# Performance work log

Measured on AMD Instinct MI355X. Metric: run time of the kernel, lower is better.

## Reference

```python
import jax, jax.numpy as jnp
import numpy as np
from jax import lax

N_EMBED, N_HEAD, N_EXPERTS, TOP_K = 1024, 16, 8, 2
D_FF = 4 * N_EMBED
HEAD = N_EMBED // N_HEAD
LN_EPS = 1e-5


def _layernorm(x, gamma, beta):
    mu = jnp.mean(x, axis=-1, keepdims=True)
    var = jnp.var(x, axis=-1, keepdims=True)
    return (x - mu) * lax.rsqrt(var + LN_EPS) * gamma + beta


def setup_inputs() -> dict:
    key = jax.random.key(0)
    ks = jax.random.split(key, 16)
    B, T = 2, 2048
    s = 0.02
    return {
        "x": jax.random.normal(ks[0], (B, T, N_EMBED), jnp.float32),
        "noise": jax.random.normal(ks[1], (B, T, N_EXPERTS), jnp.float32),
        "gamma1": jnp.ones((N_EMBED,), jnp.float32),
        "beta1": jnp.zeros((N_EMBED,), jnp.float32),
        "gamma2": jnp.ones((N_EMBED,), jnp.float32),
        "beta2": jnp.zeros((N_EMBED,), jnp.float32),
        "w_qkv": jax.random.normal(ks[2], (N_EMBED, 3 * N_EMBED), jnp.float32) * s,
        "w_out": jax.random.normal(ks[3], (N_EMBED, N_EMBED), jnp.float32) * s,
        "w_route": jax.random.normal(ks[4], (N_EMBED, N_EXPERTS), jnp.float32) * s,
        "b_route": jnp.zeros((N_EXPERTS,), jnp.float32),
        "w_noise": jax.random.normal(ks[5], (N_EMBED, N_EXPERTS), jnp.float32) * s,
        "b_noise": jnp.zeros((N_EXPERTS,), jnp.float32),
        "w1": jax.random.normal(ks[6], (N_EXPERTS, N_EMBED, D_FF), jnp.float32) * s,
        "b1": jnp.zeros((N_EXPERTS, D_FF), jnp.float32),
        "w2": jax.random.normal(ks[7], (N_EXPERTS, D_FF, N_EMBED), jnp.float32) * s,
        "b2": jnp.zeros((N_EXPERTS, N_EMBED), jnp.float32),
    }


def _attention(h, w_qkv, w_out):
    B, T, C = h.shape
    qkv = (h @ w_qkv).reshape(B, T, 3, N_HEAD, HEAD)
    q, k, v = qkv[:, :, 0], qkv[:, :, 1], qkv[:, :, 2]  # (B,T,H,hd)
    scores = jnp.einsum("bthd,bshd->bhts", q, k) / jnp.sqrt(jnp.float32(HEAD))
    attn = jax.nn.softmax(scores, axis=-1)
    out = jnp.einsum("bhts,bshd->bthd", attn, v)  # (B,T,H,hd)
    # faithful reproduction of the original permute/reshape/permute sequence
    out = jnp.transpose(out, (0, 2, 1, 3)).reshape(B, C, T)
    out = jnp.transpose(out, (0, 2, 1))  # (B,T,C)
    return out @ w_out


def _sparse_moe(h, noise, w_route, b_route, w_noise, b_noise, w1, b1, w2, b2):
    B, T, C = h.shape
    N = B * T
    flat = h.reshape(N, C)
    logits = flat @ w_route + b_route
    noise_logits = flat @ w_noise + b_noise
    noisy = logits + noise.reshape(N, N_EXPERTS) * jax.nn.softplus(noise_logits)
    full_probs = jax.nn.softmax(noisy, axis=-1)
    top_vals, top_idx = lax.top_k(noisy, TOP_K)  # (N,k)
    gates = jax.nn.softmax(top_vals, axis=-1)
    dense_gates = jnp.zeros((N, N_EXPERTS), flat.dtype).at[
        jnp.arange(N)[:, None], top_idx
    ].set(gates)
    cap = (N * TOP_K) // N_EXPERTS  # expert capacity, capacity_factor=1.0
    updates = jnp.zeros_like(flat)
    for i in range(N_EXPERTS):
        mask = (top_idx == i).any(axis=-1)  # (N,)
        order = jnp.argsort((~mask).astype(jnp.int32), stable=True)
        idx = order[:cap]
        valid = mask[idx]
        xi = flat[idx]  # (cap,C)
        hid = jax.nn.relu(xi @ w1[i] + b1[i])
        yo = hid @ w2[i] + b2[i]
        g = dense_gates[idx, i] * valid.astype(flat.dtype)
        updates = updates.at[idx].add(yo * g[:, None])
    moe_out = updates.reshape(B, T, C)
    entropy = -jnp.sum(full_probs * jnp.log(full_probs + 1e-8), axis=-1)
    return moe_out, entropy.mean()


def reference(x, noise, gamma1, beta1, gamma2, beta2, w_qkv, w_out,
              w_route, b_route, w_noise, b_noise, w1, b1, w2, b2):
    x = x + _attention(_layernorm(x, gamma1, beta1), w_qkv, w_out)
    moe_out, entropy_loss = _sparse_moe(_layernorm(x, gamma2, beta2), noise,
                                        w_route, b_route, w_noise, b_noise,
                                        w1, b1, w2, b2)
    return x + moe_out, entropy_loss
```

## Files before the change

kernel.cpp:

```cpp
#include <hip/hip_runtime.h>
#include <hip/hip_bf16.h>


#define TT   2048
#define NTOK 4096
#define CE   1024
#define DFF  4096
#define NE   8
#define CAP  1024

typedef __bf16 bf16;
typedef __attribute__((ext_vector_type(8))) bf16 bf16x8;
typedef __attribute__((ext_vector_type(4))) bf16 bf16x4;
typedef __attribute__((ext_vector_type(4))) float f32x4;

typedef __attribute__((address_space(1))) const void* as1_t;
typedef __attribute__((address_space(3))) void* as3_t;
__device__ __forceinline__ void gll16(const void* g, void* l) {
  __builtin_amdgcn_global_load_lds((as1_t)g, (as3_t)l, 16, 0, 0);
}

__device__ __forceinline__ void split2(float v, bf16& h, bf16& l) {
  h = (bf16)v;
  l = (bf16)(v - (float)h);
}

__global__ void zero_k(float* zp) { zp[threadIdx.x] = 0.f; }

template <bool LO>
__global__ __launch_bounds__(256) void wsplit_k(const float* __restrict__ W,
                                                bf16* __restrict__ Th,
                                                bf16* __restrict__ Tl,
                                                int K, int N, long sW, long sT) {
  __shared__ float tile[64][65];
  const int e = blockIdx.z;
  const float* Wb = W + (long)e * sW;
  bf16* Thb = Th + (long)e * sT;
  bf16* Tlb = LO ? Tl + (long)e * sT : nullptr;
  const int k0 = blockIdx.y * 64, n0 = blockIdx.x * 64;
  const int tx = threadIdx.x & 15, ty = threadIdx.x >> 4;
#pragma unroll
  for (int i = 0; i < 4; i++) {
    int kk = ty + i * 16;
    float4 v = *(const float4*)&Wb[(long)(k0 + kk) * N + n0 + tx * 4];
    tile[kk][tx * 4 + 0] = v.x;
    tile[kk][tx * 4 + 1] = v.y;
    tile[kk][tx * 4 + 2] = v.z;
    tile[kk][tx * 4 + 3] = v.w;
  }
  __syncthreads();
#pragma unroll
  for (int i = 0; i < 4; i++) {
    int nn = ty + i * 16;
    bf16x4 hv, lv;
#pragma unroll
    for (int j = 0; j < 4; j++) {
      float v = tile[tx * 4 + j][nn];
      bf16 h, l;
      split2(v, h, l);
      hv[j] = h;
      lv[j] = l;
    }
    long o = (long)(n0 + nn) * K + k0 + tx * 4;
    *(bf16x4*)(Thb + o) = hv;
    if (LO) *(bf16x4*)(Tlb + o) = lv;
  }
}

__global__ __launch_bounds__(256) void ln_k(const float* __restrict__ in,
                                            const float* __restrict__ g,
                                            const float* __restrict__ b,
                                            float* __restrict__ outf,
                                            bf16* __restrict__ outh,
                                            bf16* __restrict__ outl) {
  int row = blockIdx.x, tid = threadIdx.x;
  const float* xr = in + (long)row * CE;
  float v[4];
  float s = 0.f, s2 = 0.f;
#pragma unroll
  for (int i = 0; i < 4; i++) {
    v[i] = xr[tid + 256 * i];
    s += v[i];
    s2 += v[i] * v[i];
  }
#pragma unroll
  for (int o = 32; o; o >>= 1) {
    s += __shfl_xor(s, o);
    s2 += __shfl_xor(s2, o);
  }
  __shared__ float rs[4], rs2[4];
  int w = tid >> 6, lane = tid & 63;
  if (lane == 0) { rs[w] = s; rs2[w] = s2; }
  __syncthreads();
  s = rs[0] + rs[1] + rs[2] + rs[3];
  s2 = rs2[0] + rs2[1] + rs2[2] + rs2[3];
  float mu = s * (1.f / CE);
  float var = s2 * (1.f / CE) - mu * mu;
  float rstd = rsqrtf(var + 1e-5f);
  long rb = (long)row * CE;
#pragma unroll
  for (int i = 0; i < 4; i++) {
    int c = tid + 256 * i;
    float y = (v[i] - mu) * rstd * g[c] + b[c];
    if (outf) outf[rb + c] = y;
    bf16 h, l;
    split2(y, h, l);
    outh[rb + c] = h;
    outl[rb + c] = l;
  }
}

template <int NPASS, int EPI, bool AGATHER>
__global__ __launch_bounds__(256, 2) void gemm_k(
    const bf16* __restrict__ Ah, const bf16* __restrict__ Al,
    const bf16* __restrict__ BTh, const bf16* __restrict__ BTl,
    void* __restrict__ O0, void* __restrict__ O1, void* __restrict__ O2,
    void* __restrict__ O3, int M, int N, int K,
    const float* __restrict__ resid, const float* __restrict__ bias,
    const int* __restrict__ tokens, const int* __restrict__ counts,
    long sA, long sBT, long sC, int sBias, const bf16* __restrict__ zp) {
  constexpr int NS = (NPASS > 1) ? 2 : 1;
  __shared__ bf16 As[NS][128 * 32];
  __shared__ bf16 Bs[NS][128 * 32];
  const int e = blockIdx.z;
  const int n0 = blockIdx.x * 128, m0 = blockIdx.y * 128;
  const int tid = threadIdx.x;
  const int w = tid >> 6, lane = tid & 63, lm = lane & 15, qd = lane >> 4;
  const int wm = (w & 1) * 64, wn = (w >> 1) * 64;

  const bf16* Ab = Ah + (long)e * sA;
  const bf16* AbL = (NS > 1) ? Al + (long)e * sA : nullptr;
  const bf16* Bb = BTh + (long)e * sBT;
  const bf16* BbL = (NS > 1) ? BTl + (long)e * sBT : nullptr;

  const int srow0 = w * 32 + (lane >> 2);
  const int kc = (lane & 3) * 8;
  const int ldsB0 = (w * 128) * 8;
  const int ldsB1 = (w * 128 + 64) * 8;

  const bf16 *aP0, *aP1;
  int aStep0 = 32, aStep1 = 32;
  if (AGATHER) {
    int cnt = counts[e];
    int r0 = m0 + srow0, r1 = r0 + 16;
    int t0 = (r0 < cnt) ? tokens[e * CAP + r0] : -1;
    int t1 = (r1 < cnt) ? tokens[e * CAP + r1] : -1;
    aP0 = (t0 >= 0) ? Ab + (long)t0 * K + kc : zp + kc;
    aP1 = (t1 >= 0) ? Ab + (long)t1 * K + kc : zp + kc;
    if (t0 < 0) aStep0 = 0;
    if (t1 < 0) aStep1 = 0;
  } else {
    aP0 = Ab + (long)(m0 + srow0) * K + kc;
    aP1 = Ab + (long)(m0 + srow0 + 16) * K + kc;
  }
  const bf16* bP0 = Bb + (long)(n0 + srow0) * K + kc;
  const bf16* bP1 = Bb + (long)(n0 + srow0 + 16) * K + kc;
  const bf16* aP0L = nullptr; const bf16* aP1L = nullptr;
  const bf16* bP0L = nullptr; const bf16* bP1L = nullptr;
  if (NS > 1) {
    aP0L = AbL + (aP0 - Ab);
    aP1L = AbL + (aP1 - Ab);
    bP0L = BbL + (bP0 - Bb);
    bP1L = BbL + (bP1 - Bb);
  }

  f32x4 acc[4][4];
#pragma unroll
  for (int i = 0; i < 4; i++)
#pragma unroll
    for (int j = 0; j < 4; j++) acc[i][j] = (f32x4){0.f, 0.f, 0.f, 0.f};

  for (int k0 = 0; k0 < K; k0 += 32) {
    gll16(aP0, (char*)&As[0][0] + ldsB0 * 2);
    gll16(aP1, (char*)&As[0][0] + ldsB1 * 2);
    gll16(bP0, (char*)&Bs[0][0] + ldsB0 * 2);
    gll16(bP1, (char*)&Bs[0][0] + ldsB1 * 2);
    if (NS > 1) {
      gll16(aP0L, (char*)&As[1][0] + ldsB0 * 2);
      gll16(aP1L, (char*)&As[1][0] + ldsB1 * 2);
      gll16(bP0L, (char*)&Bs[1][0] + ldsB0 * 2);
      gll16(bP1L, (char*)&Bs[1][0] + ldsB1 * 2);
      aP0L += aStep0; aP1L += aStep1; bP0L += 32; bP1L += 32;
    }
    aP0 += aStep0; aP1 += aStep1; bP0 += 32; bP1 += 32;
    __syncthreads();
    bf16x8 af[NS][4], bfv[NS][4];
#pragma unroll
    for (int j = 0; j < 4; j++)
#pragma unroll
      for (int s = 0; s < NS; s++) {
        af[s][j] = *(const bf16x8*)&As[s][(wm + j * 16 + lm) * 32 + qd * 8];
        bfv[s][j] = *(const bf16x8*)&Bs[s][(wn + j * 16 + lm) * 32 + qd * 8];
      }
#pragma unroll
    for (int i = 0; i < 4; i++)
#pragma unroll
      for (int j = 0; j < 4; j++) {
        acc[i][j] = __builtin_amdgcn_mfma_f32_16x16x32_bf16(
            af[0][i], bfv[0][j], acc[i][j], 0, 0, 0);
        if (NPASS > 1) {
          acc[i][j] = __builtin_amdgcn_mfma_f32_16x16x32_bf16(
              af[0][i], bfv[1][j], acc[i][j], 0, 0, 0);
          acc[i][j] = __builtin_amdgcn_mfma_f32_16x16x32_bf16(
              af[1][i], bfv[0][j], acc[i][j], 0, 0, 0);
        }
      }
    __syncthreads();
  }
#pragma unroll
  for (int i = 0; i < 4; i++)
#pragma unroll
    for (int j = 0; j < 4; j++) {
      long row = m0 + wm + i * 16 + qd * 4;
      long col = n0 + wn + j * 16 + lm;
      if (EPI == 0) {
        if (col < 2048) {
          bf16* qh = (bf16*)O0;
          bf16* ql = (bf16*)O1;
#pragma unroll
          for (int r = 0; r < 4; r++) {
            bf16 h, l;
            split2(acc[i][j][r], h, l);
            qh[(row + r) * 2048 + col] = h;
            ql[(row + r) * 2048 + col] = l;
          }
        } else {
          long vd = col - 2048;
          long bb = row >> 11, t = row & 2047;
          bf16x4 hv, lv;
#pragma unroll
          for (int r = 0; r < 4; r++) {
            bf16 h, l;
            split2(acc[i][j][r], h, l);
            hv[r] = h;
            lv[r] = l;
          }
          long o = (bb * 1024 + vd) * (long)TT + t;
          *(bf16x4*)((bf16*)O2 + o) = hv;
          *(bf16x4*)((bf16*)O3 + o) = lv;
        }
      } else if (EPI == 1) {
        float* outp = (float*)O0;
#pragma unroll
        for (int r = 0; r < 4; r++)
          outp[(row + r) * N + col] = resid[(row + r) * N + col] + acc[i][j][r];
      } else if (EPI == 2) {
        bf16* hid = (bf16*)O0;
        float bv = bias[e * sBias + col];
#pragma unroll
        for (int r = 0; r < 4; r++) {
          float t = acc[i][j][r] + bv;
          hid[(long)e * sC + (row + r) * (long)N + col] =
              (bf16)(t > 0.f ? t : 0.f);
        }
      } else {
        float* eo = (float*)O0;
        float bv = bias[e * sBias + col];
#pragma unroll
        for (int r = 0; r < 4; r++)
          eo[(long)e * sC + (row + r) * (long)N + col] = acc[i][j][r] + bv;
      }
    }
}

__global__ __launch_bounds__(256, 2) void attn_k(
    const bf16* __restrict__ qkvh, const bf16* __restrict__ qkvl,
    const bf16* __restrict__ VTh, const bf16* __restrict__ VTl,
    bf16* __restrict__ attn_h, bf16* __restrict__ attn_l) {
  const int qt = blockIdx.x, h = blockIdx.y, b = blockIdx.z;
  const int tid = threadIdx.x, w = tid >> 6, lane = tid & 63;
  const int lm = lane & 15, qd = lane >> 4;
  __shared__ bf16 Ks[2][64 * 64];
  __shared__ bf16 Vs[2][64 * 64];
  __shared__ bf16 Ps[4][2][32][72];
  const long bb = (long)b * TT;

  bf16x8 qfh[2][2], qfl[2][2];
#pragma unroll
  for (int i = 0; i < 2; i++) {
    long qrow = (bb + qt * 128 + w * 32 + i * 16 + lm) * 2048 + h * 64;
#pragma unroll
    for (int kk = 0; kk < 2; kk++) {
      qfh[i][kk] = *(const bf16x8*)(qkvh + qrow + kk * 32 + qd * 8);
      qfl[i][kk] = *(const bf16x8*)(qkvl + qrow + kk * 32 + qd * 8);
    }
  }

  const int ktok = tid >> 3, dc = tid & 7;
  const int kws = ktok * 64 + ((dc ^ (ktok & 7)) * 8);
  const long gK0 = (bb + ktok) * 2048 + 1024 + h * 64 + dc * 8;
  const int vd = tid >> 3, tc = tid & 7;
  const int vws = vd * 64 + ((tc ^ (vd & 7)) * 8);
  const long gV0 = ((long)b * 1024 + h * 64 + vd) * (long)TT + tc * 8;

  const bf16* pKh = qkvh + gK0;
  const bf16* pKl = qkvl + gK0;
  const bf16* pVh = VTh + gV0;
  const bf16* pVl = VTl + gV0;

  float4 rkh0, rkh1, rkl0, rkl1, rvh0, rvh1, rvl0, rvl1;
#define LOADT()                                     \
  do {                                              \
    rkh0 = *(const float4*)(pKh);                   \
    rkh1 = *(const float4*)(pKh + 32 * 2048);       \
    rkl0 = *(const float4*)(pKl);                   \
    rkl1 = *(const float4*)(pKl + 32 * 2048);       \
    rvh0 = *(const float4*)(pVh);                   \
    rvh1 = *(const float4*)(pVh + 32 * TT);         \
    rvl0 = *(const float4*)(pVl);                   \
    rvl1 = *(const float4*)(pVl + 32 * TT);         \
  } while (0)
  LOADT();

  float m_i[2][4], l_i[2][4];
  f32x4 o[2][4];
#pragma unroll
  for (int i = 0; i < 2; i++)
#pragma unroll
    for (int r = 0; r < 4; r++) { m_i[i][r] = -1e30f; l_i[i][r] = 0.f; }
#pragma unroll
  for (int i = 0; i < 2; i++)
#pragma unroll
    for (int nt = 0; nt < 4; nt++) o[i][nt] = (f32x4){0.f, 0.f, 0.f, 0.f};

  const float SC = 0.125f * 1.4426950408889634f;

  for (int kt = 0; kt < TT / 64; kt++) {
    __syncthreads();
    *(float4*)&Ks[0][kws] = rkh0;
    *(float4*)&Ks[0][kws + 32 * 64] = rkh1;
    *(float4*)&Ks[1][kws] = rkl0;
    *(float4*)&Ks[1][kws + 32 * 64] = rkl1;
    *(float4*)&Vs[0][vws] = rvh0;
    *(float4*)&Vs[0][vws + 32 * 64] = rvh1;
    *(float4*)&Vs[1][vws] = rvl0;
    *(float4*)&Vs[1][vws + 32 * 64] = rvl1;
    if (kt != TT / 64 - 1) {
      pKh += 64 * 2048; pKl += 64 * 2048; pVh += 64; pVl += 64;
      LOADT();
    }
    __syncthreads();
    f32x4 sv[2][4];
#pragma unroll
    for (int i = 0; i < 2; i++)
#pragma unroll
      for (int nt = 0; nt < 4; nt++) {
        f32x4 s4 = (f32x4){0.f, 0.f, 0.f, 0.f};
        int tok = nt * 16 + lm;
#pragma unroll
        for (int kk = 0; kk < 2; kk++) {
          int slot = ((kk * 4 + qd) ^ (lm & 7)) * 8;
          bf16x8 kh = *(const bf16x8*)&Ks[0][tok * 64 + slot];
          bf16x8 kl = *(const bf16x8*)&Ks[1][tok * 64 + slot];
          s4 = __builtin_amdgcn_mfma_f32_16x16x32_bf16(qfh[i][kk], kh, s4, 0, 0, 0);
          s4 = __builtin_amdgcn_mfma_f32_16x16x32_bf16(qfh[i][kk], kl, s4, 0, 0, 0);
          s4 = __builtin_amdgcn_mfma_f32_16x16x32_bf16(qfl[i][kk], kh, s4, 0, 0, 0);
        }
        sv[i][nt] = s4 * SC;
      }
    float alpha[2][4];
#pragma unroll
    for (int i = 0; i < 2; i++)
#pragma unroll
      for (int r = 0; r < 4; r++) {
        float mx = fmaxf(fmaxf(sv[i][0][r], sv[i][1][r]),
                         fmaxf(sv[i][2][r], sv[i][3][r]));
#pragma unroll
        for (int d = 8; d; d >>= 1) mx = fmaxf(mx, __shfl_xor(mx, d));
        float mn = fmaxf(m_i[i][r], mx);
        alpha[i][r] = __builtin_exp2f(m_i[i][r] - mn);
        float rsum = 0.f;
#pragma unroll
        for (int nt = 0; nt < 4; nt++) {
          float p = __builtin_exp2f(sv[i][nt][r] - mn);
          sv[i][nt][r] = p;
          rsum += p;
        }
#pragma unroll
        for (int d = 8; d; d >>= 1) rsum += __shfl_xor(rsum, d);
        l_i[i][r] = l_i[i][r] * alpha[i][r] + rsum;
        m_i[i][r] = mn;
      }
#pragma unroll
    for (int i = 0; i < 2; i++)
#pragma unroll
      for (int nt = 0; nt < 4; nt++)
#pragma unroll
        for (int r = 0; r < 4; r++) {
          bf16 hh, ll;
          split2(sv[i][nt][r], hh, ll);
          Ps[w][0][i * 16 + qd * 4 + r][nt * 16 + lm] = hh;
          Ps[w][1][i * 16 + qd * 4 + r][nt * 16 + lm] = ll;
        }
#pragma unroll
    for (int i = 0; i < 2; i++)
#pragma unroll
      for (int nt = 0; nt < 4; nt++)
#pragma unroll
        for (int r = 0; r < 4; r++) o[i][nt][r] *= alpha[i][r];
#pragma unroll
    for (int i = 0; i < 2; i++)
#pragma unroll
      for (int kc = 0; kc < 2; kc++) {
        bf16x8 ph = *(const bf16x8*)&Ps[w][0][i * 16 + lm][kc * 32 + qd * 8];
        bf16x8 pl = *(const bf16x8*)&Ps[w][1][i * 16 + lm][kc * 32 + qd * 8];
#pragma unroll
        for (int nt = 0; nt < 4; nt++) {
          int drow = nt * 16 + lm;
          int slot = ((kc * 4 + qd) ^ (lm & 7)) * 8;
          bf16x8 vh = *(const bf16x8*)&Vs[0][drow * 64 + slot];
          bf16x8 vl = *(const bf16x8*)&Vs[1][drow * 64 + slot];
          o[i][nt] = __builtin_amdgcn_mfma_f32_16x16x32_bf16(ph, vh, o[i][nt], 0, 0, 0);
          o[i][nt] = __builtin_amdgcn_mfma_f32_16x16x32_bf16(ph, vl, o[i][nt], 0, 0, 0);
          o[i][nt] = __builtin_amdgcn_mfma_f32_16x16x32_bf16(pl, vh, o[i][nt], 0, 0, 0);
        }
      }
  }
#pragma unroll
  for (int i = 0; i < 2; i++)
#pragma unroll
    for (int nt = 0; nt < 4; nt++)
#pragma unroll
      for (int r = 0; r < 4; r++) {
        int t = qt * 128 + w * 32 + i * 16 + qd * 4 + r;
        int d = nt * 16 + lm;
        int ttn = (t & 31) * 64 + d;
        int c = h * 64 + (t >> 5);
        float v = o[i][nt][r] / l_i[i][r];
        bf16 hh, ll;
        split2(v, hh, ll);
        long idx = (bb + ttn) * (long)CE + c;
        attn_h[idx] = hh;
        attn_l[idx] = ll;
      }
#undef LOADT
}

__global__ __launch_bounds__(64) void route_k(
    const float* __restrict__ hln, const float* __restrict__ noise,
    const float* __restrict__ wr, const float* __restrict__ br,
    const float* __restrict__ wn, const float* __restrict__ bn,
    int* __restrict__ top_e, float* __restrict__ gates,
    float* __restrict__ entb) {
  int n = blockIdx.x, lane = threadIdx.x;
  const float* hr = hln + (long)n * CE;
  float aR[NE], aN[NE];
#pragma unroll
  for (int e = 0; e < NE; e++) { aR[e] = 0.f; aN[e] = 0.f; }
  for (int i = lane; i < CE; i += 64) {
    float hv = hr[i];
#pragma unroll
    for (int e = 0; e < NE; e++) {
      aR[e] += hv * wr[i * NE + e];
      aN[e] += hv * wn[i * NE + e];
    }
  }
#pragma unroll
  for (int e = 0; e < NE; e++)
#pragma unroll
    for (int d = 32; d; d >>= 1) {
      aR[e] += __shfl_xor(aR[e], d);
      aN[e] += __shfl_xor(aN[e], d);
    }
  if (lane == 0) {
    float ns[NE];
#pragma unroll
    for (int e = 0; e < NE; e++) {
      float lg = aR[e] + br[e];
      float nl = aN[e] + bn[e];
      float sp = (nl > 20.f) ? nl : log1pf(expf(nl));
      ns[e] = lg + noise[(long)n * NE + e] * sp;
    }
    int i0 = 0;
#pragma unroll
    for (int e = 1; e < NE; e++)
      if (ns[e] > ns[i0]) i0 = e;
    int i1 = (i0 == 0) ? 1 : 0;
#pragma unroll
    for (int e = 0; e < NE; e++)
      if (e != i0 && ns[e] > ns[i1]) i1 = e;
    float v0 = ns[i0], v1 = ns[i1];
    float e1v = expf(v1 - v0);
    float inv2 = 1.f / (1.f + e1v);
    top_e[2 * n] = i0;
    top_e[2 * n + 1] = i1;
    gates[2 * n] = inv2;
    gates[2 * n + 1] = e1v * inv2;
    float ssum = 0.f, p[NE];
#pragma unroll
    for (int e = 0; e < NE; e++) {
      p[e] = expf(ns[e] - v0);
      ssum += p[e];
    }
    float is = 1.f / ssum, ent = 0.f;
#pragma unroll
    for (int e = 0; e < NE; e++) {
      float pe = p[e] * is;
      ent -= pe * logf(pe + 1e-8f);
    }
    entb[n] = ent;
  }
}

__global__ __launch_bounds__(256) void assign_k(const int* __restrict__ top_e,
                                                int* __restrict__ tokens,
                                                int* __restrict__ slots,
                                                int* __restrict__ counts) {
  int e = blockIdx.x, tid = threadIdx.x, w = tid >> 6, lane = tid & 63;
  __shared__ int wtot[4];
  int basec = 0;
  for (int c = 0; c < 16; c++) {
    int n = c * 256 + tid;
    int e0 = top_e[2 * n], e1 = top_e[2 * n + 1];
    bool flag = (e0 == e) || (e1 == e);
    int rank = (e0 == e) ? 0 : 1;
    unsigned long long mask = __ballot(flag);
    int pre = __popcll(mask & ((1ull << lane) - 1ull));
    if (lane == 0) wtot[w] = __popcll(mask);
    __syncthreads();
    int wbase = basec;
    for (int i = 0; i < w; i++) wbase += wtot[i];
    if (flag) {
      int slot = wbase + pre;
      if (slot < CAP) {
        tokens[e * CAP + slot] = n;
        slots[2 * n + rank] = slot;
      } else {
        slots[2 * n + rank] = -1;
      }
    }
    int tot = wtot[0] + wtot[1] + wtot[2] + wtot[3];
    __syncthreads();
    basec += tot;
  }
  if (tid == 0) counts[e] = basec < CAP ? basec : CAP;
}

__global__ __launch_bounds__(256) void gather_k(
    float* __restrict__ outp, const float* __restrict__ eo,
    const int* __restrict__ top_e, const float* __restrict__ gates,
    const int* __restrict__ slots) {
  int n = blockIdx.x, tid = threadIdx.x;
  int e0 = top_e[2 * n], e1 = top_e[2 * n + 1];
  int s0 = slots[2 * n], s1 = slots[2 * n + 1];
  float g0 = gates[2 * n], g1 = gates[2 * n + 1];
  const float* r0 = (s0 >= 0) ? eo + ((long)e0 * CAP + s0) * CE : nullptr;
  const float* r1 = (s1 >= 0) ? eo + ((long)e1 * CAP + s1) * CE : nullptr;
  float* orow = outp + (long)n * CE;
  for (int i = tid; i < CE; i += 256) {
    float v = orow[i];
    if (r0) v += g0 * r0[i];
    if (r1) v += g1 * r1[i];
    orow[i] = v;
  }
}

__global__ __launch_bounds__(256) void entropy_k(const float* __restrict__ entb,
                                                 float* __restrict__ outp) {
  int tid = threadIdx.x;
  float s = 0.f;
  for (int i = tid; i < NTOK; i += 256) s += entb[i];
#pragma unroll
  for (int d = 32; d; d >>= 1) s += __shfl_xor(s, d);
  __shared__ float rs[4];
  int w = tid >> 6, lane = tid & 63;
  if (lane == 0) rs[w] = s;
  __syncthreads();
  if (tid == 0)
    outp[(long)NTOK * CE] = (rs[0] + rs[1] + rs[2] + rs[3]) * (1.f / NTOK);
}

extern "C" void kernel_launch(void* const* d_in, const int* in_sizes, int n_in,
                              void* d_out, int out_size, void* d_ws,
                              size_t ws_size, hipStream_t stream) {
  const float* x = (const float*)d_in[0];
  const float* noise = (const float*)d_in[1];
  const float* gamma1 = (const float*)d_in[2];
  const float* beta1 = (const float*)d_in[3];
  const float* gamma2 = (const float*)d_in[4];
  const float* beta2 = (const float*)d_in[5];
  const float* w_qkv = (const float*)d_in[6];
  const float* w_out = (const float*)d_in[7];
  const float* w_route = (const float*)d_in[8];
  const float* b_route = (const float*)d_in[9];
  const float* w_noise = (const float*)d_in[10];
  const float* b_noise = (const float*)d_in[11];
  const float* w1 = (const float*)d_in[12];
  const float* b1 = (const float*)d_in[13];
  const float* w2 = (const float*)d_in[14];
  const float* b2 = (const float*)d_in[15];
  float* out = (float*)d_out;

  char* ws = (char*)d_ws;
  size_t offA = 0;
  bf16* qkvh = (bf16*)(ws + offA);  offA += (size_t)NTOK * 2048 * 2;
  bf16* qkvl = (bf16*)(ws + offA);  offA += (size_t)NTOK * 2048 * 2;
  bf16* VTh = (bf16*)(ws + offA);   offA += (size_t)2 * 1024 * TT * 2;
  bf16* VTl = (bf16*)(ws + offA);   offA += (size_t)2 * 1024 * TT * 2;
  size_t attn_off = offA;
  bf16* attn_h = (bf16*)(ws + offA); offA += (size_t)NTOK * CE * 2;
  bf16* attn_l = (bf16*)(ws + offA); offA += (size_t)NTOK * CE * 2;
  bf16* hid = (bf16*)ws;
  float* h2f = (float*)(ws + attn_off);
  size_t szA = offA;
  size_t offB = szA;
  bf16* h1h = (bf16*)(ws + offB);    offB += (size_t)NTOK * CE * 2;
  bf16* h1l = (bf16*)(ws + offB);    offB += (size_t)NTOK * CE * 2;
  bf16* wqkvTh = (bf16*)(ws + offB); offB += (size_t)3072 * 1024 * 2;
  bf16* wqkvTl = (bf16*)(ws + offB); offB += (size_t)3072 * 1024 * 2;
  bf16* woutTh = (bf16*)(ws + offB); offB += (size_t)1024 * 1024 * 2;
  bf16* woutTl = (bf16*)(ws + offB); offB += (size_t)1024 * 1024 * 2;
  bf16* h2h = (bf16*)(ws + szA);
  bf16* h2l = (bf16*)(ws + szA + (size_t)NTOK * CE * 2);
  float* eo = (float*)(ws + szA);
  size_t offC = offB;
  bf16* w1T = (bf16*)(ws + offC);
  bf16* w2T = w1T;
  offC += (size_t)NE * DFF * CE * 2;
  size_t offS = offC;
  int* top_e = (int*)(ws + offS);   offS += (size_t)NTOK * 2 * 4;
  float* gates = (float*)(ws + offS); offS += (size_t)NTOK * 2 * 4;
  int* slots = (int*)(ws + offS);   offS += (size_t)NTOK * 2 * 4;
  int* toks = (int*)(ws + offS);    offS += (size_t)NE * CAP * 4;
  int* counts = (int*)(ws + offS);  offS += 256;
  float* entb = (float*)(ws + offS); offS += (size_t)NTOK * 4;
  float* zp = (float*)(ws + offS);  offS += 256;
  if (offS > ws_size) return;

  zero_k<<<1, 64, 0, stream>>>(zp);
  wsplit_k<true><<<dim3(48, 16, 1), 256, 0, stream>>>(w_qkv, wqkvTh, wqkvTl,
                                                      1024, 3072, 0, 0);
  wsplit_k<true><<<dim3(16, 16, 1), 256, 0, stream>>>(w_out, woutTh, woutTl,
                                                      1024, 1024, 0, 0);
  wsplit_k<false><<<dim3(64, 16, 8), 256, 0, stream>>>(
      w1, w1T, nullptr, 1024, DFF, (long)CE * DFF, (long)DFF * CE);
  ln_k<<<NTOK, 256, 0, stream>>>(x, gamma1, beta1, nullptr, h1h, h1l);
  gemm_k<3, 0, false><<<dim3(24, 32, 1), 256, 0, stream>>>(
      h1h, h1l, wqkvTh, wqkvTl, qkvh, qkvl, VTh, VTl, NTOK, 3 * CE, CE,
      nullptr, nullptr, nullptr, nullptr, 0, 0, 0, 0, (const bf16*)zp);
  attn_k<<<dim3(16, 16, 2), 256, 0, stream>>>(qkvh, qkvl, VTh, VTl, attn_h,
                                              attn_l);
  gemm_k<3, 1, false><<<dim3(8, 32, 1), 256, 0, stream>>>(
      attn_h, attn_l, woutTh, woutTl, out, nullptr, nullptr, nullptr, NTOK, CE,
      CE, x, nullptr, nullptr, nullptr, 0, 0, 0, 0, (const bf16*)zp);
  ln_k<<<NTOK, 256, 0, stream>>>(out, gamma2, beta2, h2f, h2h, h2l);
  route_k<<<NTOK, 64, 0, stream>>>(h2f, noise, w_route, b_route, w_noise,
                                   b_noise, top_e, gates, entb);
  assign_k<<<NE, 256, 0, stream>>>(top_e, toks, slots, counts);
  gemm_k<1, 2, true><<<dim3(DFF / 128, CAP / 128, NE), 256, 0, stream>>>(
      h2h, nullptr, w1T, nullptr, hid, nullptr, nullptr, nullptr, CAP, DFF, CE,
      nullptr, b1, toks, counts, 0, (long)DFF * CE, (long)CAP * DFF, DFF,
      (const bf16*)zp);
  wsplit_k<false><<<dim3(16, 64, 8), 256, 0, stream>>>(
      w2, w2T, nullptr, DFF, CE, (long)DFF * CE, (long)CE * DFF);
  gemm_k<1, 3, false><<<dim3(CE / 128, CAP / 128, NE), 256, 0, stream>>>(
      hid, nullptr, w2T, nullptr, eo, nullptr, nullptr, nullptr, CAP, CE, DFF,
      nullptr, b2, nullptr, nullptr, (long)CAP * DFF, (long)CE * DFF,
      (long)CAP * CE, CE, (const bf16*)zp);
  gather_k<<<NTOK, 256, 0, stream>>>(out, eo, top_e, gates, slots);
  entropy_k<<<1, 256, 0, stream>>>(entb, out);
}
```

Measured before the change: 983.4 us.

## Fuse MoE combine into FFN2 epilogue, drop online softmax max, retile out-proj GEMM

Several changes land together. The second expert GEMM now scatters gated results straight into the output with atomicAdd, which removes the expert-output buffer and the separate gather kernel. Attention drops the running-max online softmax and exponentiates raw scaled scores, saving the max reductions and rescales but risking overflow for large logits. The V transpose/split moves out of the QKV GEMM epilogue into a new kernel, the out-projection GEMM uses 64-row tiles for more blocks, and the zero-init kernel is folded into the first layernorm.

```diff
diff --git a/kernel.cpp b/kernel.cpp
--- a/kernel.cpp
+++ b/kernel.cpp
@@ -24,8 +24,6 @@
   h = (bf16)v;
   l = (bf16)(v - (float)h);
 }
-
-__global__ void zero_k(float* zp) { zp[threadIdx.x] = 0.f; }
 
 template <bool LO>
 __global__ __launch_bounds__(256) void wsplit_k(const float* __restrict__ W,
@@ -67,13 +65,50 @@
   }
 }
 
+__global__ __launch_bounds__(256) void vsplit_k(const float* __restrict__ V,
+                                                bf16* __restrict__ Th,
+                                                bf16* __restrict__ Tl) {
+  __shared__ float tile[64][65];
+  const int b = blockIdx.z;
+  const int vd0 = blockIdx.x * 64, t0 = blockIdx.y * 64;
+  const int tx = threadIdx.x & 15, ty = threadIdx.x >> 4;
+#pragma unroll
+  for (int i = 0; i < 4; i++) {
+    int tt = ty + i * 16;
+    float4 v = *(const float4*)&V[((long)b * TT + t0 + tt) * 1024 + vd0 + tx * 4];
+    tile[tt][tx * 4 + 0] = v.x;
+    tile[tt][tx * 4 + 1] = v.y;
+    tile[tt][tx * 4 + 2] = v.z;
+    tile[tt][tx * 4 + 3] = v.w;
+  }
+  __syncthreads();
+#pragma unroll
+  for (int i = 0; i < 4; i++) {
+    int vd = ty + i * 16;
+    bf16x4 hv, lv;
+#pragma unroll
+    for (int j = 0; j < 4; j++) {
+      float v = tile[tx * 4 + j][vd];
+      bf16 h, l;
+      split2(v, h, l);
+      hv[j] = h;
+      lv[j] = l;
+    }
+    long o = ((long)b * 1024 + vd0 + vd) * (long)TT + t0 + tx * 4;
+    *(bf16x4*)(Th + o) = hv;
+    *(bf16x4*)(Tl + o) = lv;
+  }
+}
+
 __global__ __launch_bounds__(256) void ln_k(const float* __restrict__ in,
                                             const float* __restrict__ g,
                                             const float* __restrict__ b,
                                             float* __restrict__ outf,
                                             bf16* __restrict__ outh,
-                                            bf16* __restrict__ outl) {
+                                            bf16* __restrict__ outl,
+                                            float* __restrict__ zp) {
   int row = blockIdx.x, tid = threadIdx.x;
+  if (zp && row == 0 && tid < 64) zp[tid] = 0.f;
   const float* xr = in + (long)row * CE;
   float v[4];
   float s = 0.f, s2 = 0.f;
@@ -110,90 +145,100 @@
   }
 }
 
-template <int NPASS, int EPI, bool AGATHER>
+template <int NPASS, int EPI, bool AGATHER, int TM>
 __global__ __launch_bounds__(256, 2) void gemm_k(
     const bf16* __restrict__ Ah, const bf16* __restrict__ Al,
     const bf16* __restrict__ BTh, const bf16* __restrict__ BTl,
     void* __restrict__ O0, void* __restrict__ O1, void* __restrict__ O2,
-    void* __restrict__ O3, int M, int N, int K,
-    const float* __restrict__ resid, const float* __restrict__ bias,
-    const int* __restrict__ tokens, const int* __restrict__ counts,
+    int M, int N, int K, const float* __restrict__ resid,
+    const float* __restrict__ bias, const int* __restrict__ tokens,
+    const int* __restrict__ counts, const float* __restrict__ gslot,
     long sA, long sBT, long sC, int sBias, const bf16* __restrict__ zp) {
   constexpr int NS = (NPASS > 1) ? 2 : 1;
-  __shared__ bf16 As[NS][128 * 32];
+  constexpr int MI = TM / 32;
+  constexpr int AISS = TM / 64;
+  __shared__ bf16 As[NS][TM * 32];
   __shared__ bf16 Bs[NS][128 * 32];
   const int e = blockIdx.z;
-  const int n0 = blockIdx.x * 128, m0 = blockIdx.y * 128;
+  const int n0 = blockIdx.x * 128, m0 = blockIdx.y * TM;
   const int tid = threadIdx.x;
   const int w = tid >> 6, lane = tid & 63, lm = lane & 15, qd = lane >> 4;
-  const int wm = (w & 1) * 64, wn = (w >> 1) * 64;
+  const int wm = (w & 1) * (TM / 2), wn = (w >> 1) * 64;
 
   const bf16* Ab = Ah + (long)e * sA;
   const bf16* AbL = (NS > 1) ? Al + (long)e * sA : nullptr;
   const bf16* Bb = BTh + (long)e * sBT;
   const bf16* BbL = (NS > 1) ? BTl + (long)e * sBT : nullptr;
 
-  const int srow0 = w * 32 + (lane >> 2);
   const int kc = (lane & 3) * 8;
-  const int ldsB0 = (w * 128) * 8;
-  const int ldsB1 = (w * 128 + 64) * 8;
-
-  const bf16 *aP0, *aP1;
-  int aStep0 = 32, aStep1 = 32;
-  if (AGATHER) {
-    int cnt = counts[e];
-    int r0 = m0 + srow0, r1 = r0 + 16;
-    int t0 = (r0 < cnt) ? tokens[e * CAP + r0] : -1;
-    int t1 = (r1 < cnt) ? tokens[e * CAP + r1] : -1;
-    aP0 = (t0 >= 0) ? Ab + (long)t0 * K + kc : zp + kc;
-    aP1 = (t1 >= 0) ? Ab + (long)t1 * K + kc : zp + kc;
-    if (t0 < 0) aStep0 = 0;
-    if (t1 < 0) aStep1 = 0;
-  } else {
-    aP0 = Ab + (long)(m0 + srow0) * K + kc;
-    aP1 = Ab + (long)(m0 + srow0 + 16) * K + kc;
-  }
-  const bf16* bP0 = Bb + (long)(n0 + srow0) * K + kc;
-  const bf16* bP1 = Bb + (long)(n0 + srow0 + 16) * K + kc;
-  const bf16* aP0L = nullptr; const bf16* aP1L = nullptr;
-  const bf16* bP0L = nullptr; const bf16* bP1L = nullptr;
-  if (NS > 1) {
-    aP0L = AbL + (aP0 - Ab);
-    aP1L = AbL + (aP1 - Ab);
-    bP0L = BbL + (bP0 - Bb);
-    bP1L = BbL + (bP1 - Bb);
-  }
-
-  f32x4 acc[4][4];
-#pragma unroll
-  for (int i = 0; i < 4; i++)
+  int cnt = 0;
+  if (AGATHER || EPI == 3) cnt = counts[e];
+
+  const bf16* aP[AISS];
+  const bf16* aPL[AISS];
+  int aStep[AISS];
+  int ldsA[AISS];
+#pragma unroll
+  for (int ii = 0; ii < AISS; ii++) {
+    int sr = w * (TM / 4) + ii * 16 + (lane >> 2);
+    ldsA[ii] = (w * TM + ii * 64) * 8;
+    aStep[ii] = 32;
+    if (AGATHER) {
+      int gm = m0 + sr;
+      int tk = (gm < cnt) ? tokens[e * CAP + gm] : -1;
+      if (tk < 0) { aP[ii] = (const bf16*)zp + kc; aStep[ii] = 0; }
+      else aP[ii] = Ab + (long)tk * K + kc;
+    } else {
+      aP[ii] = Ab + (long)(m0 + sr) * K + kc;
+    }
+    aPL[ii] = (NS > 1) ? AbL + (aP[ii] - Ab) : nullptr;
+  }
+  const bf16* bP[2];
+  const bf16* bPL[2];
+  int ldsB[2];
+#pragma unroll
+  for (int ii = 0; ii < 2; ii++) {
+    int sr = w * 32 + ii * 16 + (lane >> 2);
+    ldsB[ii] = (w * 128 + ii * 64) * 8;
+    bP[ii] = Bb + (long)(n0 + sr) * K + kc;
+    bPL[ii] = (NS > 1) ? BbL + (bP[ii] - Bb) : nullptr;
+  }
+
+  f32x4 acc[MI][4];
+#pragma unroll
+  for (int i = 0; i < MI; i++)
 #pragma unroll
     for (int j = 0; j < 4; j++) acc[i][j] = (f32x4){0.f, 0.f, 0.f, 0.f};
 
   for (int k0 = 0; k0 < K; k0 += 32) {
-    gll16(aP0, (char*)&As[0][0] + ldsB0 * 2);
-    gll16(aP1, (char*)&As[0][0] + ldsB1 * 2);
-    gll16(bP0, (char*)&Bs[0][0] + ldsB0 * 2);
-    gll16(bP1, (char*)&Bs[0][0] + ldsB1 * 2);
-    if (NS > 1) {
-      gll16(aP0L, (char*)&As[1][0] + ldsB0 * 2);
-      gll16(aP1L, (char*)&As[1][0] + ldsB1 * 2);
-      gll16(bP0L, (char*)&Bs[1][0] + ldsB0 * 2);
-      gll16(bP1L, (char*)&Bs[1][0] + ldsB1 * 2);
-      aP0L += aStep0; aP1L += aStep1; bP0L += 32; bP1L += 32;
-    }
-    aP0 += aStep0; aP1 += aStep1; bP0 += 32; bP1 += 32;
+#pragma unroll
+    for (int ii = 0; ii < AISS; ii++) {
+      gll16(aP[ii], (char*)&As[0][0] + ldsA[ii] * 2);
+      if (NS > 1) gll16(aPL[ii], (char*)&As[1][0] + ldsA[ii] * 2);
+      aP[ii] += aStep[ii];
+      if (NS > 1) aPL[ii] += aStep[ii];
+    }
+#pragma unroll
+    for (int ii = 0; ii < 2; ii++) {
+      gll16(bP[ii], (char*)&Bs[0][0] + ldsB[ii] * 2);
+      if (NS > 1) gll16(bPL[ii], (char*)&Bs[1][0] + ldsB[ii] * 2);
+      bP[ii] += 32;
+      if (NS > 1) bPL[ii] += 32;
+    }
     __syncthreads();
-    bf16x8 af[NS][4], bfv[NS][4];
+    bf16x8 af[NS][MI], bfv[NS][4];
 #pragma unroll
     for (int j = 0; j < 4; j++)
 #pragma unroll
-      for (int s = 0; s < NS; s++) {
-        af[s][j] = *(const bf16x8*)&As[s][(wm + j * 16 + lm) * 32 + qd * 8];
+      for (int s = 0; s < NS; s++)
         bfv[s][j] = *(const bf16x8*)&Bs[s][(wn + j * 16 + lm) * 32 + qd * 8];
-      }
-#pragma unroll
-    for (int i = 0; i < 4; i++)
+#pragma unroll
+    for (int i = 0; i < MI; i++)
+#pragma unroll
+      for (int s = 0; s < NS; s++)
+        af[s][i] = *(const bf16x8*)&As[s][(wm + i * 16 + lm) * 32 + qd * 8];
+#pragma unroll
+    for (int i = 0; i < MI; i++)
 #pragma unroll
       for (int j = 0; j < 4; j++) {
         acc[i][j] = __builtin_amdgcn_mfma_f32_16x16x32_bf16(
@@ -208,7 +253,7 @@
     __syncthreads();
   }
 #pragma unroll
-  for (int i = 0; i < 4; i++)
+  for (int i = 0; i < MI; i++)
 #pragma unroll
     for (int j = 0; j < 4; j++) {
       long row = m0 + wm + i * 16 + qd * 4;
@@ -225,19 +270,10 @@
             ql[(row + r) * 2048 + col] = l;
           }
         } else {
+          float* vt = (float*)O2;
           long vd = col - 2048;
-          long bb = row >> 11, t = row & 2047;
-          bf16x4 hv, lv;
-#pragma unroll
-          for (int r = 0; r < 4; r++) {
-            bf16 h, l;
-            split2(acc[i][j][r], h, l);
-            hv[r] = h;
-            lv[r] = l;
-          }
-          long o = (bb * 1024 + vd) * (long)TT + t;
-          *(bf16x4*)((bf16*)O2 + o) = hv;
-          *(bf16x4*)((bf16*)O3 + o) = lv;
+#pragma unroll
+          for (int r = 0; r < 4; r++) vt[(row + r) * 1024 + vd] = acc[i][j][r];
         }
       } else if (EPI == 1) {
         float* outp = (float*)O0;
@@ -254,11 +290,17 @@
               (bf16)(t > 0.f ? t : 0.f);
         }
       } else {
-        float* eo = (float*)O0;
+        float* outp = (float*)O0;
         float bv = bias[e * sBias + col];
 #pragma unroll
-        for (int r = 0; r < 4; r++)
-          eo[(long)e * sC + (row + r) * (long)N + col] = acc[i][j][r] + bv;
+        for (int r = 0; r < 4; r++) {
+          long rr = row + r;
+          if (rr < cnt) {
+            int tok = tokens[e * CAP + rr];
+            float gv = gslot[e * CAP + rr];
+            atomicAdd(&outp[(long)tok * CE + col], gv * (acc[i][j][r] + bv));
+          }
+        }
       }
     }
 }
@@ -299,25 +341,25 @@
   const bf16* pVl = VTl + gV0;
 
   float4 rkh0, rkh1, rkl0, rkl1, rvh0, rvh1, rvl0, rvl1;
-#define LOADT()                                     \
-  do {                                              \
-    rkh0 = *(const float4*)(pKh);                   \
-    rkh1 = *(const float4*)(pKh + 32 * 2048);       \
-    rkl0 = *(const float4*)(pKl);                   \
-    rkl1 = *(const float4*)(pKl + 32 * 2048);       \
-    rvh0 = *(const float4*)(pVh);                   \
-    rvh1 = *(const float4*)(pVh + 32 * TT);         \
-    rvl0 = *(const float4*)(pVl);                   \
-    rvl1 = *(const float4*)(pVl + 32 * TT);         \
+#define LOADT()                               \
+  do {                                        \
+    rkh0 = *(const float4*)(pKh);             \
+    rkh1 = *(const float4*)(pKh + 32 * 2048); \
+    rkl0 = *(const float4*)(pKl);             \
+    rkl1 = *(const float4*)(pKl + 32 * 2048); \
+    rvh0 = *(const float4*)(pVh);             \
+    rvh1 = *(const float4*)(pVh + 32 * TT);   \
+    rvl0 = *(const float4*)(pVl);             \
+    rvl1 = *(const float4*)(pVl + 32 * TT);   \
   } while (0)
   LOADT();
 
-  float m_i[2][4], l_i[2][4];
+  float l_lane[2][4];
   f32x4 o[2][4];
 #pragma unroll
   for (int i = 0; i < 2; i++)
 #pragma unroll
-    for (int r = 0; r < 4; r++) { m_i[i][r] = -1e30f; l_i[i][r] = 0.f; }
+    for (int r = 0; r < 4; r++) l_lane[i][r] = 0.f;
 #pragma unroll
   for (int i = 0; i < 2; i++)
 #pragma unroll
@@ -344,78 +386,68 @@
 #pragma unroll
     for (int i = 0; i < 2; i++)
 #pragma unroll
-      for (int nt = 0; nt < 4; nt++) {
-        f32x4 s4 = (f32x4){0.f, 0.f, 0.f, 0.f};
-        int tok = nt * 16 + lm;
-#pragma unroll
-        for (int kk = 0; kk < 2; kk++) {
-          int slot = ((kk * 4 + qd) ^ (lm & 7)) * 8;
-          bf16x8 kh = *(const bf16x8*)&Ks[0][tok * 64 + slot];
-          bf16x8 kl = *(const bf16x8*)&Ks[1][tok * 64 + slot];
-          s4 = __builtin_amdgcn_mfma_f32_16x16x32_bf16(qfh[i][kk], kh, s4, 0, 0, 0);
-          s4 = __builtin_amdgcn_mfma_f32_16x16x32_bf16(qfh[i][kk], kl, s4, 0, 0, 0);
-          s4 = __builtin_amdgcn_mfma_f32_16x16x32_bf16(qfl[i][kk], kh, s4, 0, 0, 0);
+      for (int nt = 0; nt < 4; nt++) sv[i][nt] = (f32x4){0.f, 0.f, 0.f, 0.f};
+#pragma unroll
+    for (int nt = 0; nt < 4; nt++) {
+      int tok = nt * 16 + lm;
+#pragma unroll
+      for (int kk = 0; kk < 2; kk++) {
+        int slot = ((kk * 4 + qd) ^ (lm & 7)) * 8;
+        bf16x8 kh = *(const bf16x8*)&Ks[0][tok * 64 + slot];
+        bf16x8 kl = *(const bf16x8*)&Ks[1][tok * 64 + slot];
+#pragma unroll
+        for (int i = 0; i < 2; i++) {
+          sv[i][nt] = __builtin_amdgcn_mfma_f32_16x16x32_bf16(qfh[i][kk], kh,
+                                                              sv[i][nt], 0, 0, 0);
+          sv[i][nt] = __builtin_amdgcn_mfma_f32_16x16x32_bf16(qfh[i][kk], kl,
+                                                              sv[i][nt], 0, 0, 0);
+          sv[i][nt] = __builtin_amdgcn_mfma_f32_16x16x32_bf16(qfl[i][kk], kh,
+                                                              sv[i][nt], 0, 0, 0);
         }
-        sv[i][nt] = s4 * SC;
       }
-    float alpha[2][4];
+    }
 #pragma unroll
     for (int i = 0; i < 2; i++)
 #pragma unroll
-      for (int r = 0; r < 4; r++) {
-        float mx = fmaxf(fmaxf(sv[i][0][r], sv[i][1][r]),
-                         fmaxf(sv[i][2][r], sv[i][3][r]));
-#pragma unroll
-        for (int d = 8; d; d >>= 1) mx = fmaxf(mx, __shfl_xor(mx, d));
-        float mn = fmaxf(m_i[i][r], mx);
-        alpha[i][r] = __builtin_exp2f(m_i[i][r] - mn);
-        float rsum = 0.f;
-#pragma unroll
-        for (int nt = 0; nt < 4; nt++) {
-          float p = __builtin_exp2f(sv[i][nt][r] - mn);
-          sv[i][nt][r] = p;
-          rsum += p;
-        }
-#pragma unroll
-        for (int d = 8; d; d >>= 1) rsum += __shfl_xor(rsum, d);
-        l_i[i][r] = l_i[i][r] * alpha[i][r] + rsum;
-        m_i[i][r] = mn;
-      }
-#pragma unroll
-    for (int i = 0; i < 2; i++)
-#pragma unroll
       for (int nt = 0; nt < 4; nt++)
 #pragma unroll
         for (int r = 0; r < 4; r++) {
+          float p = __builtin_exp2f(sv[i][nt][r] * SC);
+          l_lane[i][r] += p;
           bf16 hh, ll;
-          split2(sv[i][nt][r], hh, ll);
+          split2(p, hh, ll);
           Ps[w][0][i * 16 + qd * 4 + r][nt * 16 + lm] = hh;
           Ps[w][1][i * 16 + qd * 4 + r][nt * 16 + lm] = ll;
         }
 #pragma unroll
-    for (int i = 0; i < 2; i++)
-#pragma unroll
-      for (int nt = 0; nt < 4; nt++)
-#pragma unroll
-        for (int r = 0; r < 4; r++) o[i][nt][r] *= alpha[i][r];
-#pragma unroll
-    for (int i = 0; i < 2; i++)
-#pragma unroll
-      for (int kc = 0; kc < 2; kc++) {
-        bf16x8 ph = *(const bf16x8*)&Ps[w][0][i * 16 + lm][kc * 32 + qd * 8];
-        bf16x8 pl = *(const bf16x8*)&Ps[w][1][i * 16 + lm][kc * 32 + qd * 8];
-#pragma unroll
-        for (int nt = 0; nt < 4; nt++) {
-          int drow = nt * 16 + lm;
-          int slot = ((kc * 4 + qd) ^ (lm & 7)) * 8;
-          bf16x8 vh = *(const bf16x8*)&Vs[0][drow * 64 + slot];
-          bf16x8 vl = *(const bf16x8*)&Vs[1][drow * 64 + slot];
-          o[i][nt] = __builtin_amdgcn_mfma_f32_16x16x32_bf16(ph, vh, o[i][nt], 0, 0, 0);
-          o[i][nt] = __builtin_amdgcn_mfma_f32_16x16x32_bf16(ph, vl, o[i][nt], 0, 0, 0);
-          o[i][nt] = __builtin_amdgcn_mfma_f32_16x16x32_bf16(pl, vh, o[i][nt], 0, 0, 0);
+    for (int kcl = 0; kcl < 2; kcl++) {
+      bf16x8 ph[2], pl[2];
+#pragma unroll
+      for (int i = 0; i < 2; i++) {
+        ph[i] = *(const bf16x8*)&Ps[w][0][i * 16 + lm][kcl * 32 + qd * 8];
+        pl[i] = *(const bf16x8*)&Ps[w][1][i * 16 + lm][kcl * 32 + qd * 8];
+      }
+#pragma unroll
+      for (int nt = 0; nt < 4; nt++) {
+        int drow = nt * 16 + lm;
+        int slot = ((kcl * 4 + qd) ^ (lm & 7)) * 8;
+        bf16x8 vh = *(const bf16x8*)&Vs[0][drow * 64 + slot];
+        bf16x8 vl = *(const bf16x8*)&Vs[1][drow * 64 + slot];
+#pragma unroll
+        for (int i = 0; i < 2; i++) {
+          o[i][nt] = __builtin_amdgcn_mfma_f32_16x16x32_bf16(ph[i], vh, o[i][nt], 0, 0, 0);
+          o[i][nt] = __builtin_amdgcn_mfma_f32_16x16x32_bf16(ph[i], vl, o[i][nt], 0, 0, 0);
+          o[i][nt] = __builtin_amdgcn_mfma_f32_16x16x32_bf16(pl[i], vh, o[i][nt], 0, 0, 0);
         }
       }
-  }
+    }
+  }
+#pragma unroll
+  for (int i = 0; i < 2; i++)
+#pragma unroll
+    for (int r = 0; r < 4; r++)
+#pragma unroll
+      for (int d = 8; d; d >>= 1) l_lane[i][r] += __shfl_xor(l_lane[i][r], d);
 #pragma unroll
   for (int i = 0; i < 2; i++)
 #pragma unroll
@@ -426,7 +458,7 @@
         int d = nt * 16 + lm;
         int ttn = (t & 31) * 64 + d;
         int c = h * 64 + (t >> 5);
-        float v = o[i][nt][r] / l_i[i][r];
+        float v = o[i][nt][r] / l_lane[i][r];
         bf16 hh, ll;
         split2(v, hh, ll);
         long idx = (bb + ttn) * (long)CE + c;
@@ -503,8 +535,9 @@
 }
 
 __global__ __launch_bounds__(256) void assign_k(const int* __restrict__ top_e,
+                                                const float* __restrict__ gates,
                                                 int* __restrict__ tokens,
-                                                int* __restrict__ slots,
+                                                float* __restrict__ gslot,
                                                 int* __restrict__ counts) {
   int e = blockIdx.x, tid = threadIdx.x, w = tid >> 6, lane = tid & 63;
   __shared__ int wtot[4];
@@ -524,9 +557,7 @@
       int slot = wbase + pre;
       if (slot < CAP) {
         tokens[e * CAP + slot] = n;
-        slots[2 * n + rank] = slot;
-      } else {
-        slots[2 * n + rank] = -1;
+        gslot[e * CAP + slot] = gates[2 * n + rank];
       }
     }
     int tot = wtot[0] + wtot[1] + wtot[2] + wtot[3];
@@ -534,25 +565,6 @@
     basec += tot;
   }
   if (tid == 0) counts[e] = basec < CAP ? basec : CAP;
-}
-
-__global__ __launch_bounds__(256) void gather_k(
-    float* __restrict__ outp, const float* __restrict__ eo,
-    const int* __restrict__ top_e, const float* __restrict__ gates,
-    const int* __restrict__ slots) {
-  int n = blockIdx.x, tid = threadIdx.x;
-  int e0 = top_e[2 * n], e1 = top_e[2 * n + 1];
-  int s0 = slots[2 * n], s1 = slots[2 * n + 1];
-  float g0 = gates[2 * n], g1 = gates[2 * n + 1];
-  const float* r0 = (s0 >= 0) ? eo + ((long)e0 * CAP + s0) * CE : nullptr;
-  const float* r1 = (s1 >= 0) ? eo + ((long)e1 * CAP + s1) * CE : nullptr;
-  float* orow = outp + (long)n * CE;
-  for (int i = tid; i < CE; i += 256) {
-    float v = orow[i];
-    if (r0) v += g0 * r0[i];
-    if (r1) v += g1 * r1[i];
-    orow[i] = v;
-  }
 }
 
 __global__ __launch_bounds__(256) void entropy_k(const float* __restrict__ entb,
@@ -601,6 +613,7 @@
   bf16* attn_h = (bf16*)(ws + offA); offA += (size_t)NTOK * CE * 2;
   bf16* attn_l = (bf16*)(ws + offA); offA += (size_t)NTOK * CE * 2;
   bf16* hid = (bf16*)ws;
+  float* vtmp = (float*)(ws + attn_off);
   float* h2f = (float*)(ws + attn_off);
   size_t szA = offA;
   size_t offB = szA;
@@ -612,51 +625,49 @@
   bf16* woutTl = (bf16*)(ws + offB); offB += (size_t)1024 * 1024 * 2;
   bf16* h2h = (bf16*)(ws + szA);
   bf16* h2l = (bf16*)(ws + szA + (size_t)NTOK * CE * 2);
-  float* eo = (float*)(ws + szA);
   size_t offC = offB;
   bf16* w1T = (bf16*)(ws + offC);
   bf16* w2T = w1T;
   offC += (size_t)NE * DFF * CE * 2;
   size_t offS = offC;
-  int* top_e = (int*)(ws + offS);   offS += (size_t)NTOK * 2 * 4;
+  int* top_e = (int*)(ws + offS);    offS += (size_t)NTOK * 2 * 4;
   float* gates = (float*)(ws + offS); offS += (size_t)NTOK * 2 * 4;
-  int* slots = (int*)(ws + offS);   offS += (size_t)NTOK * 2 * 4;
-  int* toks = (int*)(ws + offS);    offS += (size_t)NE * CAP * 4;
-  int* counts = (int*)(ws + offS);  offS += 256;
+  int* toks = (int*)(ws + offS);     offS += (size_t)NE * CAP * 4;
+  float* gslot = (float*)(ws + offS); offS += (size_t)NE * CAP * 4;
+  int* counts = (int*)(ws + offS);   offS += 256;
   float* entb = (float*)(ws + offS); offS += (size_t)NTOK * 4;
-  float* zp = (float*)(ws + offS);  offS += 256;
+  float* zp = (float*)(ws + offS);   offS += 256;
   if (offS > ws_size) return;
 
-  zero_k<<<1, 64, 0, stream>>>(zp);
   wsplit_k<true><<<dim3(48, 16, 1), 256, 0, stream>>>(w_qkv, wqkvTh, wqkvTl,
                                                       1024, 3072, 0, 0);
   wsplit_k<true><<<dim3(16, 16, 1), 256, 0, stream>>>(w_out, woutTh, woutTl,
                                                       1024, 1024, 0, 0);
   wsplit_k<false><<<dim3(64, 16, 8), 256, 0, stream>>>(
       w1, w1T, nullptr, 1024, DFF, (long)CE * DFF, (long)DFF * CE);
-  ln_k<<<NTOK, 256, 0, stream>>>(x, gamma1, beta1, nullptr, h1h, h1l);
-  gemm_k<3, 0, false><<<dim3(24, 32, 1), 256, 0, stream>>>(
-      h1h, h1l, wqkvTh, wqkvTl, qkvh, qkvl, VTh, VTl, NTOK, 3 * CE, CE,
+  ln_k<<<NTOK, 256, 0, stream>>>(x, gamma1, beta1, nullptr, h1h, h1l, zp);
+  gemm_k<3, 0, false, 128><<<dim3(24, 32, 1), 256, 0, stream>>>(
+      h1h, h1l, wqkvTh, wqkvTl, qkvh, qkvl, vtmp, NTOK, 3 * CE, CE, nullptr,
       nullptr, nullptr, nullptr, nullptr, 0, 0, 0, 0, (const bf16*)zp);
+  vsplit_k<<<dim3(16, 32, 2), 256, 0, stream>>>(vtmp, VTh, VTl);
   attn_k<<<dim3(16, 16, 2), 256, 0, stream>>>(qkvh, qkvl, VTh, VTl, attn_h,
                                               attn_l);
-  gemm_k<3, 1, false><<<dim3(8, 32, 1), 256, 0, stream>>>(
-      attn_h, attn_l, woutTh, woutTl, out, nullptr, nullptr, nullptr, NTOK, CE,
-      CE, x, nullptr, nullptr, nullptr, 0, 0, 0, 0, (const bf16*)zp);
-  ln_k<<<NTOK, 256, 0, stream>>>(out, gamma2, beta2, h2f, h2h, h2l);
+  gemm_k<3, 1, false, 64><<<dim3(8, 64, 1), 256, 0, stream>>>(
+      attn_h, attn_l, woutTh, woutTl, out, nullptr, nullptr, NTOK, CE, CE, x,
+      nullptr, nullptr, nullptr, nullptr, 0, 0, 0, 0, (const bf16*)zp);
+  ln_k<<<NTOK, 256, 0, stream>>>(out, gamma2, beta2, h2f, h2h, h2l, nullptr);
   route_k<<<NTOK, 64, 0, stream>>>(h2f, noise, w_route, b_route, w_noise,
                                    b_noise, top_e, gates, entb);
-  assign_k<<<NE, 256, 0, stream>>>(top_e, toks, slots, counts);
-  gemm_k<1, 2, true><<<dim3(DFF / 128, CAP / 128, NE), 256, 0, stream>>>(
-      h2h, nullptr, w1T, nullptr, hid, nullptr, nullptr, nullptr, CAP, DFF, CE,
-      nullptr, b1, toks, counts, 0, (long)DFF * CE, (long)CAP * DFF, DFF,
+  assign_k<<<NE, 256, 0, stream>>>(top_e, gates, toks, gslot, counts);
+  gemm_k<1, 2, true, 128><<<dim3(DFF / 128, CAP / 128, NE), 256, 0, stream>>>(
+      h2h, nullptr, w1T, nullptr, hid, nullptr, nullptr, CAP, DFF, CE, nullptr,
+      b1, toks, counts, nullptr, 0, (long)DFF * CE, (long)CAP * DFF, DFF,
       (const bf16*)zp);
   wsplit_k<false><<<dim3(16, 64, 8), 256, 0, stream>>>(
       w2, w2T, nullptr, DFF, CE, (long)DFF * CE, (long)CE * DFF);
-  gemm_k<1, 3, false><<<dim3(CE / 128, CAP / 128, NE), 256, 0, stream>>>(
-      hid, nullptr, w2T, nullptr, eo, nullptr, nullptr, nullptr, CAP, CE, DFF,
-      nullptr, b2, nullptr, nullptr, (long)CAP * DFF, (long)CE * DFF,
-      (long)CAP * CE, CE, (const bf16*)zp);
-  gather_k<<<NTOK, 256, 0, stream>>>(out, eo, top_e, gates, slots);
+  gemm_k<1, 3, false, 128><<<dim3(CE / 128, CAP / 128, NE), 256, 0, stream>>>(
+      hid, nullptr, w2T, nullptr, out, nullptr, nullptr, CAP, CE, DFF, nullptr,
+      b2, toks, counts, gslot, (long)CAP * DFF, (long)CE * DFF, 0, CE,
+      (const bf16*)zp);
   entropy_k<<<1, 256, 0, stream>>>(entb, out);
 }
```

Result: faster. 913.5 us (-7.1%).
